# Performance work log

Hardware: AMD Instinct MI355X
Metric: run time of the kernel (lower is better)

Reference implementation:

```python
import jax, jax.numpy as jnp
import numpy as np

NS = 150            # number of MC weight samples
D_IN, D_H, D_OUT = 1024, 512, 256


def setup_inputs() -> dict:
    key = jax.random.key(0)
    ks = jax.random.split(key, 9)
    x = jax.random.normal(ks[0], (32, D_IN), dtype=jnp.float32)
    # variational means (mu network params)
    mu_W1 = jax.random.normal(ks[1], (D_H, D_IN), dtype=jnp.float32) * 0.02
    mu_b1 = jnp.zeros((D_H,), dtype=jnp.float32)
    mu_W2 = jax.random.normal(ks[2], (D_OUT, D_H), dtype=jnp.float32) * 0.02
    mu_b2 = jnp.zeros((D_OUT,), dtype=jnp.float32)
    # variational log-stds (std network params v); std = exp(v)
    v_W1 = -3.0 + 0.1 * jax.random.normal(ks[3], (D_H, D_IN), dtype=jnp.float32)
    v_b1 = -3.0 + 0.1 * jax.random.normal(ks[4], (D_H,), dtype=jnp.float32)
    v_W2 = -3.0 + 0.1 * jax.random.normal(ks[5], (D_OUT, D_H), dtype=jnp.float32)
    v_b2 = -3.0 + 0.1 * jax.random.normal(ks[6], (D_OUT,), dtype=jnp.float32)
    return {
        "x": x,
        "mu_W1": mu_W1, "mu_b1": mu_b1, "mu_W2": mu_W2, "mu_b2": mu_b2,
        "v_W1": v_W1, "v_b1": v_b1, "v_W2": v_W2, "v_b2": v_b2,
    }


def reference(x, mu_W1, mu_b1, mu_W2, mu_b2, v_W1, v_b1, v_W2, v_b2):
    # Reparameterization: w = mu + eps * sqrt(exp(2v)) = mu + eps * exp(v)
    nk = jax.random.split(jax.random.key(42), 4)
    eW1 = jax.random.normal(nk[0], (NS,) + mu_W1.shape, dtype=mu_W1.dtype)
    eb1 = jax.random.normal(nk[1], (NS,) + mu_b1.shape, dtype=mu_b1.dtype)
    eW2 = jax.random.normal(nk[2], (NS,) + mu_W2.shape, dtype=mu_W2.dtype)
    eb2 = jax.random.normal(nk[3], (NS,) + mu_b2.shape, dtype=mu_b2.dtype)

    W1 = mu_W1 + eW1 * jnp.exp(v_W1)          # [ns, H, I]
    b1 = mu_b1 + eb1 * jnp.exp(v_b1)          # [ns, H]
    W2 = mu_W2 + eW2 * jnp.exp(v_W2)          # [ns, O, H]
    b2 = mu_b2 + eb2 * jnp.exp(v_b2)          # [ns, O]

    # MLP forward, batched over the ns sample axis
    h = jax.nn.relu(jnp.einsum('bi,nhi->nbh', x, W1) + b1[:, None, :])  # [ns, B, H]
    y = jnp.einsum('nbh,noh->nbo', h, W2) + b2[:, None, :]              # [ns, B, O]
    return y  # stacked MC outputs, [ns, B, O]
```

## Files before the change

kernel.cpp:

```cpp
#include <hip/hip_runtime.h>
#include <stdint.h>

#define NS 150
#define D_IN 1024
#define D_H 512
#define D_OUT 256

typedef __bf16 bf16x8 __attribute__((ext_vector_type(8)));
typedef float f32x4 __attribute__((ext_vector_type(4)));

#define OFF_XF    0u
#define OFF_MS1T  16384u
#define OFF_MS2T  1064960u
#define OFF_B1S   1327104u
#define OFF_B2S   1403904u
#define OFF_HB    1442304u

#define ROTL32(x, r) __builtin_rotateleft32((x), (r))

__host__ __device__ __forceinline__ void threefry2x32(uint32_t k0, uint32_t k1,
                                                      uint32_t x0, uint32_t x1,
                                                      uint32_t& o0, uint32_t& o1) {
  uint32_t k2 = k0 ^ k1 ^ 0x1BD11BDAu;
  x0 += k0; x1 += k1;
#define TFR(r) { x0 += x1; x1 = ROTL32(x1, r); x1 ^= x0; }
  TFR(13) TFR(15) TFR(26) TFR(6)
  x0 += k1; x1 += k2 + 1u;
  TFR(17) TFR(29) TFR(16) TFR(24)
  x0 += k2; x1 += k0 + 2u;
  TFR(13) TFR(15) TFR(26) TFR(6)
  x0 += k0; x1 += k1 + 3u;
  TFR(17) TFR(29) TFR(16) TFR(24)
  x0 += k1; x1 += k2 + 4u;
  TFR(13) TFR(15) TFR(26) TFR(6)
  x0 += k2; x1 += k0 + 5u;
#undef TFR
  o0 = x0; o1 = x1;
}

__device__ __forceinline__ float tf_normal(uint32_t k0, uint32_t k1, uint32_t idx) {
  uint32_t o0, o1;
  threefry2x32(k0, k1, 0u, idx, o0, o1);
  uint32_t bits = o0 ^ o1;
  uint32_t fb = (bits >> 9) | 0x3F800000u;
  float m = __uint_as_float(fb);
  const float lo = -0.99999994f;
  float u = fmaxf(fmaf(m, 2.0f, -3.0f), lo);
  float t = fmaf(u, -u, 1.0f);
  float w = -0.69314718056f * __builtin_amdgcn_logf(t);
  const float S = 1.41421354f;
  float p;
  if (w < 5.0f) {
    float ww = w - 2.5f;
    p = S * 2.81022636e-08f;
    p = fmaf(p, ww, S * 3.43273939e-07f);
    p = fmaf(p, ww, S * -3.5233877e-06f);
    p = fmaf(p, ww, S * -4.39150654e-06f);
    p = fmaf(p, ww, S * 0.00021858087f);
    p = fmaf(p, ww, S * -0.00125372503f);
    p = fmaf(p, ww, S * -0.00417768164f);
    p = fmaf(p, ww, S * 0.246640727f);
    p = fmaf(p, ww, S * 1.50140941f);
  } else {
    float ww = __builtin_amdgcn_sqrtf(w) - 3.0f;
    p = S * -0.000200214257f;
    p = fmaf(p, ww, S * 0.000100950558f);
    p = fmaf(p, ww, S * 0.00134934322f);
    p = fmaf(p, ww, S * -0.00367342844f);
    p = fmaf(p, ww, S * 0.00573950773f);
    p = fmaf(p, ww, S * -0.0076224613f);
    p = fmaf(p, ww, S * 0.00943887047f);
    p = fmaf(p, ww, S * 1.00167406f);
    p = fmaf(p, ww, S * 2.83297682f);
  }
  return p * u;
}

#define TF_ADD8 \
  "v_add_u32 %[a0], %[a0], %[b0]\n\t" "v_add_u32 %[a1], %[a1], %[b1]\n\t" \
  "v_add_u32 %[a2], %[a2], %[b2]\n\t" "v_add_u32 %[a3], %[a3], %[b3]\n\t" \
  "v_add_u32 %[a4], %[a4], %[b4]\n\t" "v_add_u32 %[a5], %[a5], %[b5]\n\t" \
  "v_add_u32 %[a6], %[a6], %[b6]\n\t" "v_add_u32 %[a7], %[a7], %[b7]\n\t"
#define TF_ROT8(sh) \
  "v_alignbit_b32 %[b0], %[b0], %[b0], " sh "\n\t" \
  "v_alignbit_b32 %[b1], %[b1], %[b1], " sh "\n\t" \
  "v_alignbit_b32 %[b2], %[b2], %[b2], " sh "\n\t" \
  "v_alignbit_b32 %[b3], %[b3], %[b3], " sh "\n\t" \
  "v_alignbit_b32 %[b4], %[b4], %[b4], " sh "\n\t" \
  "v_alignbit_b32 %[b5], %[b5], %[b5], " sh "\n\t" \
  "v_alignbit_b32 %[b6], %[b6], %[b6], " sh "\n\t" \
  "v_alignbit_b32 %[b7], %[b7], %[b7], " sh "\n\t"
#define TF_XOR8 \
  "v_xor_b32 %[b0], %[b0], %[a0]\n\t" "v_xor_b32 %[b1], %[b1], %[a1]\n\t" \
  "v_xor_b32 %[b2], %[b2], %[a2]\n\t" "v_xor_b32 %[b3], %[b3], %[a3]\n\t" \
  "v_xor_b32 %[b4], %[b4], %[a4]\n\t" "v_xor_b32 %[b5], %[b5], %[a5]\n\t" \
  "v_xor_b32 %[b6], %[b6], %[a6]\n\t" "v_xor_b32 %[b7], %[b7], %[a7]\n\t"
#define TF_ROUND(sh) TF_ADD8 TF_ROT8(sh) TF_XOR8
#define TF_INJ(KA, KB) \
  "v_add_u32 %[a0], " KA ", %[a0]\n\t" "v_add_u32 %[a1], " KA ", %[a1]\n\t" \
  "v_add_u32 %[a2], " KA ", %[a2]\n\t" "v_add_u32 %[a3], " KA ", %[a3]\n\t" \
  "v_add_u32 %[a4], " KA ", %[a4]\n\t" "v_add_u32 %[a5], " KA ", %[a5]\n\t" \
  "v_add_u32 %[a6], " KA ", %[a6]\n\t" "v_add_u32 %[a7], " KA ", %[a7]\n\t" \
  "v_add_u32 %[b0], " KB ", %[b0]\n\t" "v_add_u32 %[b1], " KB ", %[b1]\n\t" \
  "v_add_u32 %[b2], " KB ", %[b2]\n\t" "v_add_u32 %[b3], " KB ", %[b3]\n\t" \
  "v_add_u32 %[b4], " KB ", %[b4]\n\t" "v_add_u32 %[b5], " KB ", %[b5]\n\t" \
  "v_add_u32 %[b6], " KB ", %[b6]\n\t" "v_add_u32 %[b7], " KB ", %[b7]\n\t"

__device__ __forceinline__ void tf8_bits(uint32_t k0, uint32_t k1, uint32_t k2,
                                         uint32_t idx0, uint32_t* bits) {
  uint32_t k2p1 = k2 + 1u, k0p2 = k0 + 2u, k1p3 = k1 + 3u;
  uint32_t k2p4 = k2 + 4u, k0p5 = k0 + 5u;
  uint32_t t0 = idx0 + k1;
  uint32_t a0 = k0, a1 = k0, a2 = k0, a3 = k0, a4 = k0, a5 = k0, a6 = k0, a7 = k0;
  uint32_t b0 = t0, b1 = t0 + 1u, b2 = t0 + 2u, b3 = t0 + 3u;
  uint32_t b4 = t0 + 4u, b5 = t0 + 5u, b6 = t0 + 6u, b7 = t0 + 7u;
  asm(TF_ROUND("19") TF_ROUND("17") TF_ROUND("6") TF_ROUND("26")
      TF_INJ("%[k1]", "%[k2p1]")
      TF_ROUND("15") TF_ROUND("3") TF_ROUND("16") TF_ROUND("8")
      TF_INJ("%[k2]", "%[k0p2]")
      TF_ROUND("19") TF_ROUND("17") TF_ROUND("6") TF_ROUND("26")
      TF_INJ("%[k0]", "%[k1p3]")
      TF_ROUND("15") TF_ROUND("3") TF_ROUND("16") TF_ROUND("8")
      TF_INJ("%[k1]", "%[k2p4]")
      TF_ROUND("19") TF_ROUND("17") TF_ROUND("6") TF_ROUND("26")
      TF_INJ("%[k2]", "%[k0p5]")
      : [a0]"+v"(a0), [a1]"+v"(a1), [a2]"+v"(a2), [a3]"+v"(a3),
        [a4]"+v"(a4), [a5]"+v"(a5), [a6]"+v"(a6), [a7]"+v"(a7),
        [b0]"+v"(b0), [b1]"+v"(b1), [b2]"+v"(b2), [b3]"+v"(b3),
        [b4]"+v"(b4), [b5]"+v"(b5), [b6]"+v"(b6), [b7]"+v"(b7)
      : [k0]"s"(k0), [k1]"s"(k1), [k2]"s"(k2), [k2p1]"s"(k2p1),
        [k0p2]"s"(k0p2), [k1p3]"s"(k1p3), [k2p4]"s"(k2p4), [k0p5]"s"(k0p5));
  bits[0] = a0 ^ b0; bits[1] = a1 ^ b1; bits[2] = a2 ^ b2; bits[3] = a3 ^ b3;
  bits[4] = a4 ^ b4; bits[5] = a5 ^ b5; bits[6] = a6 ^ b6; bits[7] = a7 ^ b7;
}

__device__ __forceinline__ float bits_normal(uint32_t bits) {
  uint32_t fb = (bits >> 9) | 0x3F800000u;
  float m = __uint_as_float(fb);
  const float lo = -0.99999994f;
  float u = fmaxf(fmaf(m, 2.0f, -3.0f), lo);
  float t = fmaf(u, -u, 1.0f);
  float w = -0.69314718056f * __builtin_amdgcn_logf(t);
  const float S = 1.41421354f;
  float p;
  if (w < 5.0f) {
    float ww = w - 2.5f;
    p = S * 2.81022636e-08f;
    p = fmaf(p, ww, S * 3.43273939e-07f);
    p = fmaf(p, ww, S * -3.5233877e-06f);
    p = fmaf(p, ww, S * -4.39150654e-06f);
    p = fmaf(p, ww, S * 0.00021858087f);
    p = fmaf(p, ww, S * -0.00125372503f);
    p = fmaf(p, ww, S * -0.00417768164f);
    p = fmaf(p, ww, S * 0.246640727f);
    p = fmaf(p, ww, S * 1.50140941f);
  } else {
    float ww = __builtin_amdgcn_sqrtf(w) - 3.0f;
    p = S * -0.000200214257f;
    p = fmaf(p, ww, S * 0.000100950558f);
    p = fmaf(p, ww, S * 0.00134934322f);
    p = fmaf(p, ww, S * -0.00367342844f);
    p = fmaf(p, ww, S * 0.00573950773f);
    p = fmaf(p, ww, S * -0.0076224613f);
    p = fmaf(p, ww, S * 0.00943887047f);
    p = fmaf(p, ww, S * 1.00167406f);
    p = fmaf(p, ww, S * 2.83297682f);
  }
  return p * u;
}

__global__ __launch_bounds__(256) void prep_kernel(
    const float* __restrict__ x,
    const float* __restrict__ muW1, const float* __restrict__ vW1,
    const float* __restrict__ muW2, const float* __restrict__ vW2,
    const float* __restrict__ mub1, const float* __restrict__ vb1,
    const float* __restrict__ mub2, const float* __restrict__ vb2,
    float* __restrict__ ws,
    uint32_t kb1_0, uint32_t kb1_1, uint32_t kb2_0, uint32_t kb2_1) {
  int bb = blockIdx.x;
  int tid = threadIdx.x;
  if (bb < 2048) {
    int t = bb * 256 + tid;
    ((float2*)(ws + OFF_MS1T))[t] = make_float2(muW1[t], expf(vW1[t]));
  } else if (bb < 2560) {
    int t = (bb - 2048) * 256 + tid;
    ((float2*)(ws + OFF_MS2T))[t] = make_float2(muW2[t], expf(vW2[t]));
  } else if (bb < 2688) {
    int t = (bb - 2560) * 256 + tid;
    int j = t & 7, lane = (t >> 3) & 63, fidx = t >> 9;
    int s = fidx >> 1, f = fidx & 1;
    int b = f * 16 + (lane & 15);
    int k = s * 32 + ((lane >> 4) << 3) + j;
    ((__bf16*)(ws + OFF_XF))[t] = (__bf16)x[b * D_IN + k];
  } else if (bb < 2988) {
    int t = (bb - 2688) * 256 + tid;
    int h = t & 511;
    float eps = tf_normal(kb1_0, kb1_1, (uint32_t)t);
    ws[OFF_B1S + t] = fmaf(eps, expf(vb1[h]), mub1[h]);
  } else {
    int t = (bb - 2988) * 256 + tid;
    int o = t & 255;
    float eps = tf_normal(kb2_0, kb2_1, (uint32_t)t);
    ws[OFF_B2S + t] = fmaf(eps, expf(vb2[o]), mub2[o]);
  }
}

__global__ __launch_bounds__(256) void l1_kernel(
    const float* __restrict__ ws, uint32_t k0, uint32_t k1) {
  const float2* __restrict__ ms1 = (const float2*)(ws + OFF_MS1T);
  const bf16x8* __restrict__ xf = (const bf16x8*)(ws + OFF_XF);
  const float* __restrict__ b1s = ws + OFF_B1S;
  __bf16* __restrict__ hB = (__bf16*)(ws + OFF_HB);
  uint32_t k2 = k0 ^ k1 ^ 0x1BD11BDAu;

  __shared__ f32x4 lred[2][2][64];

  int lane = threadIdx.x & 63;
  int wib = threadIdx.x >> 6;
  int pairIdx = wib >> 1, khalf = wib & 1;
  int tile = blockIdx.x * 2 + pairIdx;
  int n = tile >> 5;
  int ht = tile & 31;
  int mrow = lane & 15, quad = lane >> 4;
  int h = ht * 16 + mrow;
  uint32_t base = ((uint32_t)(n * 512 + h)) << 10;
  const float2* __restrict__ msrow = ms1 + (size_t)h * D_IN;

  f32x4 acc0 = {0.f, 0.f, 0.f, 0.f}, acc1 = {0.f, 0.f, 0.f, 0.f};

  int send = khalf * 16 + 16;
  for (int s = khalf * 16; s < send; ++s) {
    int kq = s * 32 + quad * 8;
    const f32x4* msq = (const f32x4*)(msrow + kq);
    f32x4 q0 = msq[0], q1 = msq[1], q2 = msq[2], q3 = msq[3];
    bf16x8 b0 = xf[(s * 2 + 0) * 64 + lane];
    bf16x8 b1 = xf[(s * 2 + 1) * 64 + lane];
    uint32_t bits[8];
    tf8_bits(k0, k1, k2, base + (uint32_t)kq, bits);
    float mu[8], sd[8];
    mu[0]=q0[0]; sd[0]=q0[1]; mu[1]=q0[2]; sd[1]=q0[3];
    mu[2]=q1[0]; sd[2]=q1[1]; mu[3]=q1[2]; sd[3]=q1[3];
    mu[4]=q2[0]; sd[4]=q2[1]; mu[5]=q2[2]; sd[5]=q2[3];
    mu[6]=q3[0]; sd[6]=q3[1]; mu[7]=q3[2]; sd[7]=q3[3];
    bf16x8 a;
#pragma unroll
    for (int j = 0; j < 8; ++j) {
      float eps = bits_normal(bits[j]);
      a[j] = (__bf16)fmaf(eps, sd[j], mu[j]);
    }
    acc0 = __builtin_amdgcn_mfma_f32_16x16x32_bf16(a, b0, acc0, 0, 0, 0);
    acc1 = __builtin_amdgcn_mfma_f32_16x16x32_bf16(a, b1, acc1, 0, 0, 0);
  }

  if (khalf) {
    lred[pairIdx][0][lane] = acc0;
    lred[pairIdx][1][lane] = acc1;
  }
  __syncthreads();
  if (!khalf) {
    f32x4 r0 = lred[pairIdx][0][lane], r1 = lred[pairIdx][1][lane];
    acc0 += r0; acc1 += r1;
    int hq = ht * 16 + quad * 4;
    float4 bias = *(const float4*)(b1s + n * 512 + hq);
    float bv[4] = {bias.x, bias.y, bias.z, bias.w};
    union { __bf16 v[4]; uint2 u; } p0, p1;
#pragma unroll
    for (int r = 0; r < 4; ++r) {
      p0.v[r] = (__bf16)fmaxf(acc0[r] + bv[r], 0.0f);
      p1.v[r] = (__bf16)fmaxf(acc1[r] + bv[r], 0.0f);
    }
    *(uint2*)(hB + ((size_t)(n * 32 + mrow) * 512 + hq)) = p0.u;
    *(uint2*)(hB + ((size_t)(n * 32 + 16 + mrow) * 512 + hq)) = p1.u;
  }
}

__global__ __launch_bounds__(256) void l2_kernel(
    const float* __restrict__ ws, float* __restrict__ y,
    uint32_t k0, uint32_t k1) {
  const float2* __restrict__ ms2 = (const float2*)(ws + OFF_MS2T);
  const bf16x8* __restrict__ hB8 = (const bf16x8*)(ws + OFF_HB);
  const float* __restrict__ b2s = ws + OFF_B2S;
  uint32_t k2 = k0 ^ k1 ^ 0x1BD11BDAu;

  __shared__ f32x4 lred[3][2][64];

  int lane = threadIdx.x & 63;
  int wib = threadIdx.x >> 6;
  int tile = blockIdx.x;
  int n = tile >> 4;
  int ot = tile & 15;
  int mrow = lane & 15, quad = lane >> 4;
  int o = ot * 16 + mrow;
  uint32_t base = (uint32_t)(n * 256 + o) << 9;
  const float2* __restrict__ msrow = ms2 + (size_t)o * D_H;

  f32x4 acc0 = {0.f, 0.f, 0.f, 0.f}, acc1 = {0.f, 0.f, 0.f, 0.f};

  int send = wib * 4 + 4;
  for (int s = wib * 4; s < send; ++s) {
    int kq = s * 32 + quad * 8;
    const f32x4* msq = (const f32x4*)(msrow + kq);
    f32x4 q0 = msq[0], q1 = msq[1], q2 = msq[2], q3 = msq[3];
    bf16x8 b0 = hB8[(size_t)(n * 32 + mrow) * 64 + s * 4 + quad];
    bf16x8 b1 = hB8[(size_t)(n * 32 + 16 + mrow) * 64 + s * 4 + quad];
    uint32_t bits[8];
    tf8_bits(k0, k1, k2, base + (uint32_t)kq, bits);
    float mu[8], sd[8];
    mu[0]=q0[0]; sd[0]=q0[1]; mu[1]=q0[2]; sd[1]=q0[3];
    mu[2]=q1[0]; sd[2]=q1[1]; mu[3]=q1[2]; sd[3]=q1[3];
    mu[4]=q2[0]; sd[4]=q2[1]; mu[5]=q2[2]; sd[5]=q2[3];
    mu[6]=q3[0]; sd[6]=q3[1]; mu[7]=q3[2]; sd[7]=q3[3];
    bf16x8 a;
#pragma unroll
    for (int j = 0; j < 8; ++j) {
      float eps = bits_normal(bits[j]);
      a[j] = (__bf16)fmaf(eps, sd[j], mu[j]);
    }
    acc0 = __builtin_amdgcn_mfma_f32_16x16x32_bf16(a, b0, acc0, 0, 0, 0);
    acc1 = __builtin_amdgcn_mfma_f32_16x16x32_bf16(a, b1, acc1, 0, 0, 0);
  }

  if (wib) {
    lred[wib - 1][0][lane] = acc0;
    lred[wib - 1][1][lane] = acc1;
  }
  __syncthreads();
  if (!wib) {
#pragma unroll
    for (int c = 0; c < 3; ++c) {
      acc0 += lred[c][0][lane];
      acc1 += lred[c][1][lane];
    }
    int oq = ot * 16 + quad * 4;
    float4 bias = *(const float4*)(b2s + n * 256 + oq);
    float4 o0, o1;
    o0.x = acc0[0] + bias.x; o0.y = acc0[1] + bias.y;
    o0.z = acc0[2] + bias.z; o0.w = acc0[3] + bias.w;
    o1.x = acc1[0] + bias.x; o1.y = acc1[1] + bias.y;
    o1.z = acc1[2] + bias.z; o1.w = acc1[3] + bias.w;
    *(float4*)(y + (size_t)(n * 32 + mrow) * 256 + oq) = o0;
    *(float4*)(y + (size_t)(n * 32 + 16 + mrow) * 256 + oq) = o1;
  }
}

extern "C" void kernel_launch(void* const* d_in, const int* in_sizes, int n_in,
                              void* d_out, int out_size, void* d_ws, size_t ws_size,
                              hipStream_t stream) {
  const float* x = (const float*)d_in[0];
  const float* muW1 = (const float*)d_in[1];
  const float* mub1 = (const float*)d_in[2];
  const float* muW2 = (const float*)d_in[3];
  const float* mub2 = (const float*)d_in[4];
  const float* vW1 = (const float*)d_in[5];
  const float* vb1 = (const float*)d_in[6];
  const float* vW2 = (const float*)d_in[7];
  const float* vb2 = (const float*)d_in[8];
  float* y = (float*)d_out;
  float* ws = (float*)d_ws;

  uint32_t nk[4][2];
  for (uint32_t j = 0; j < 4; ++j) {
    threefry2x32(0u, 42u, 0u, j, nk[j][0], nk[j][1]);
  }

  prep_kernel<<<3138, 256, 0, stream>>>(
      x, muW1, vW1, muW2, vW2, mub1, vb1, mub2, vb2, ws,
      nk[1][0], nk[1][1], nk[3][0], nk[3][1]);

  l1_kernel<<<2400, 256, 0, stream>>>(ws, nk[0][0], nk[0][1]);

  l2_kernel<<<2400, 256, 0, stream>>>(ws, y, nk[2][0], nk[2][1]);
}
```

Before: 301.4 us.

## Shorten normal-inverse polynomial in log domain and halve L2 kernel K-split

```diff
diff --git a/kernel.cpp b/kernel.cpp
--- a/kernel.cpp
+++ b/kernel.cpp
@@ -15,6 +15,38 @@
 #define OFF_B1S   1327104u
 #define OFF_B2S   1403904u
 #define OFF_HB    1442304u
+
+#define SQ2 1.41421354f
+#define CT0 (SQ2 * -0.000200214257f)
+#define CT1 (SQ2 * 0.000100950558f)
+#define CT2 (SQ2 * 0.00134934322f)
+#define CT3 (SQ2 * -0.00367342844f)
+#define CT4 (SQ2 * 0.00573950773f)
+#define CT5 (SQ2 * -0.0076224613f)
+#define CT6 (SQ2 * 0.00943887047f)
+#define CT7 (SQ2 * 0.246640727f)
+#define CM8 (SQ2 * 1.50140941f)
+
+#define DSQ2 1.4142135623730951
+#define DA  (-0.6931471805599453)
+#define ZC3 ((float)(DSQ2 * -4.39150654e-06 * DA*DA*DA*DA*DA))
+#define ZC4 ((float)(DSQ2 * 0.00021858087   * DA*DA*DA*DA))
+#define ZC5 ((float)(DSQ2 * -0.00125372503  * DA*DA*DA))
+#define ZC6 ((float)(DSQ2 * -0.00417768164  * DA*DA))
+#define ZC7 ((float)(DSQ2 * 0.246640727     * DA))
+#define ZC8 ((float)(DSQ2 * 1.50140941))
+#define ZSHIFT 3.6067376022224085f
+#define ZCUT  -7.213475204444817f
+
+#define TT0 (SQ2 * -0.000200214257f)
+#define TT1 (SQ2 * 0.000100950558f)
+#define TT2 (SQ2 * 0.00134934322f)
+#define TT3 (SQ2 * -0.00367342844f)
+#define TT4 (SQ2 * 0.00573950773f)
+#define TT5 (SQ2 * -0.0076224613f)
+#define TT6 (SQ2 * 0.00943887047f)
+#define TT7 (SQ2 * 1.00167406f)
+#define TT8 (SQ2 * 2.83297682f)
 
 #define ROTL32(x, r) __builtin_rotateleft32((x), (r))
 
@@ -48,30 +80,24 @@
   float u = fmaxf(fmaf(m, 2.0f, -3.0f), lo);
   float t = fmaf(u, -u, 1.0f);
   float w = -0.69314718056f * __builtin_amdgcn_logf(t);
-  const float S = 1.41421354f;
   float p;
   if (w < 5.0f) {
     float ww = w - 2.5f;
-    p = S * 2.81022636e-08f;
-    p = fmaf(p, ww, S * 3.43273939e-07f);
-    p = fmaf(p, ww, S * -3.5233877e-06f);
-    p = fmaf(p, ww, S * -4.39150654e-06f);
-    p = fmaf(p, ww, S * 0.00021858087f);
-    p = fmaf(p, ww, S * -0.00125372503f);
-    p = fmaf(p, ww, S * -0.00417768164f);
-    p = fmaf(p, ww, S * 0.246640727f);
-    p = fmaf(p, ww, S * 1.50140941f);
+    p = SQ2 * 2.81022636e-08f;
+    p = fmaf(p, ww, SQ2 * 3.43273939e-07f);
+    p = fmaf(p, ww, SQ2 * -3.5233877e-06f);
+    p = fmaf(p, ww, SQ2 * -4.39150654e-06f);
+    p = fmaf(p, ww, SQ2 * 0.00021858087f);
+    p = fmaf(p, ww, SQ2 * -0.00125372503f);
+    p = fmaf(p, ww, SQ2 * -0.00417768164f);
+    p = fmaf(p, ww, SQ2 * 0.246640727f);
+    p = fmaf(p, ww, SQ2 * 1.50140941f);
   } else {
     float ww = __builtin_amdgcn_sqrtf(w) - 3.0f;
-    p = S * -0.000200214257f;
-    p = fmaf(p, ww, S * 0.000100950558f);
-    p = fmaf(p, ww, S * 0.00134934322f);
-    p = fmaf(p, ww, S * -0.00367342844f);
-    p = fmaf(p, ww, S * 0.00573950773f);
-    p = fmaf(p, ww, S * -0.0076224613f);
-    p = fmaf(p, ww, S * 0.00943887047f);
-    p = fmaf(p, ww, S * 1.00167406f);
-    p = fmaf(p, ww, S * 2.83297682f);
+    p = TT0;
+    p = fmaf(p, ww, TT1); p = fmaf(p, ww, TT2); p = fmaf(p, ww, TT3);
+    p = fmaf(p, ww, TT4); p = fmaf(p, ww, TT5); p = fmaf(p, ww, TT6);
+    p = fmaf(p, ww, TT7); p = fmaf(p, ww, TT8);
   }
   return p * u;
 }
@@ -140,31 +166,20 @@
   const float lo = -0.99999994f;
   float u = fmaxf(fmaf(m, 2.0f, -3.0f), lo);
   float t = fmaf(u, -u, 1.0f);
-  float w = -0.69314718056f * __builtin_amdgcn_logf(t);
-  const float S = 1.41421354f;
+  float z = __builtin_amdgcn_logf(t);
   float p;
-  if (w < 5.0f) {
-    float ww = w - 2.5f;
-    p = S * 2.81022636e-08f;
-    p = fmaf(p, ww, S * 3.43273939e-07f);
-    p = fmaf(p, ww, S * -3.5233877e-06f);
-    p = fmaf(p, ww, S * -4.39150654e-06f);
-    p = fmaf(p, ww, S * 0.00021858087f);
-    p = fmaf(p, ww, S * -0.00125372503f);
-    p = fmaf(p, ww, S * -0.00417768164f);
-    p = fmaf(p, ww, S * 0.246640727f);
-    p = fmaf(p, ww, S * 1.50140941f);
+  if (z > ZCUT) {
+    float zz = z + ZSHIFT;
+    p = ZC3;
+    p = fmaf(p, zz, ZC4); p = fmaf(p, zz, ZC5); p = fmaf(p, zz, ZC6);
+    p = fmaf(p, zz, ZC7); p = fmaf(p, zz, ZC8);
   } else {
+    float w = -0.69314718056f * z;
     float ww = __builtin_amdgcn_sqrtf(w) - 3.0f;
-    p = S * -0.000200214257f;
-    p = fmaf(p, ww, S * 0.000100950558f);
-    p = fmaf(p, ww, S * 0.00134934322f);
-    p = fmaf(p, ww, S * -0.00367342844f);
-    p = fmaf(p, ww, S * 0.00573950773f);
-    p = fmaf(p, ww, S * -0.0076224613f);
-    p = fmaf(p, ww, S * 0.00943887047f);
-    p = fmaf(p, ww, S * 1.00167406f);
-    p = fmaf(p, ww, S * 2.83297682f);
+    p = TT0;
+    p = fmaf(p, ww, TT1); p = fmaf(p, ww, TT2); p = fmaf(p, ww, TT3);
+    p = fmaf(p, ww, TT4); p = fmaf(p, ww, TT5); p = fmaf(p, ww, TT6);
+    p = fmaf(p, ww, TT7); p = fmaf(p, ww, TT8);
   }
   return p * u;
 }
@@ -282,11 +297,12 @@
   const float* __restrict__ b2s = ws + OFF_B2S;
   uint32_t k2 = k0 ^ k1 ^ 0x1BD11BDAu;
 
-  __shared__ f32x4 lred[3][2][64];
+  __shared__ f32x4 lred[2][2][64];
 
   int lane = threadIdx.x & 63;
   int wib = threadIdx.x >> 6;
-  int tile = blockIdx.x;
+  int pairIdx = wib >> 1, khalf = wib & 1;
+  int tile = blockIdx.x * 2 + pairIdx;
   int n = tile >> 4;
   int ot = tile & 15;
   int mrow = lane & 15, quad = lane >> 4;
@@ -296,8 +312,8 @@
 
   f32x4 acc0 = {0.f, 0.f, 0.f, 0.f}, acc1 = {0.f, 0.f, 0.f, 0.f};
 
-  int send = wib * 4 + 4;
-  for (int s = wib * 4; s < send; ++s) {
+  int send = khalf * 8 + 8;
+  for (int s = khalf * 8; s < send; ++s) {
     int kq = s * 32 + quad * 8;
     const f32x4* msq = (const f32x4*)(msrow + kq);
     f32x4 q0 = msq[0], q1 = msq[1], q2 = msq[2], q3 = msq[3];
@@ -320,17 +336,14 @@
     acc1 = __builtin_amdgcn_mfma_f32_16x16x32_bf16(a, b1, acc1, 0, 0, 0);
   }
 
-  if (wib) {
-    lred[wib - 1][0][lane] = acc0;
-    lred[wib - 1][1][lane] = acc1;
+  if (khalf) {
+    lred[pairIdx][0][lane] = acc0;
+    lred[pairIdx][1][lane] = acc1;
   }
   __syncthreads();
-  if (!wib) {
-#pragma unroll
-    for (int c = 0; c < 3; ++c) {
-      acc0 += lred[c][0][lane];
-      acc1 += lred[c][1][lane];
-    }
+  if (!khalf) {
+    f32x4 r0 = lred[pairIdx][0][lane], r1 = lred[pairIdx][1][lane];
+    acc0 += r0; acc1 += r1;
     int oq = ot * 16 + quad * 4;
     float4 bias = *(const float4*)(b2s + n * 256 + oq);
     float4 o0, o1;
@@ -369,5 +382,5 @@
 
   l1_kernel<<<2400, 256, 0, stream>>>(ws, nk[0][0], nk[0][1]);
 
-  l2_kernel<<<2400, 256, 0, stream>>>(ws, y, nk[2][0], nk[2][1]);
-}
+  l2_kernel<<<1200, 256, 0, stream>>>(ws, y, nk[2][0], nk[2][1]);
+}
```

New measurement: 297.8 us. About the same (-1.2%).
